# Kernel optimization log

Measured on AMD Instinct MI355X. Metric: run time of the kernel, lower is better.

## Reference

```python
import jax, jax.numpy as jnp
import numpy as np

DIM = 512
HEADS = 16
DIM_HEAD = 64
INNER = HEADS * DIM_HEAD
MAX_T = 32
BASE = 10000.0


def rotate_half(t):
    t1, t2 = jnp.split(t, 2, axis=-1)
    return jnp.concatenate((-t2, t1), axis=-1)


def setup_inputs() -> dict:
    key = jax.random.key(0)
    ks = jax.random.split(key, 12)
    B, T, S = 2, 16, 128
    x = jax.random.normal(ks[0], (B, T, S, DIM), dtype=jnp.float32)
    y = jax.random.normal(ks[1], (B, T, S, DIM), dtype=jnp.float32)
    temporal_mask = jax.random.randint(ks[2], (B, T, T), 0, 2).astype(jnp.int32)
    sc = 1.0 / np.sqrt(DIM)
    Wq = jax.random.normal(ks[3], (DIM, INNER), dtype=jnp.float32) * sc
    Wk = jax.random.normal(ks[4], (DIM, INNER), dtype=jnp.float32) * sc
    Wv = jax.random.normal(ks[5], (DIM, INNER), dtype=jnp.float32) * sc
    Wo = jax.random.normal(ks[6], (INNER, DIM), dtype=jnp.float32) / np.sqrt(INNER)
    bo = jnp.zeros((DIM,), dtype=jnp.float32)
    pos_emb = jax.random.normal(ks[7], (MAX_T, DIM), dtype=jnp.float32)
    gate_w = jax.random.normal(ks[8], (DIM, 1), dtype=jnp.float32) * sc
    gate_b = jnp.zeros((1,), dtype=jnp.float32)
    return {"x": x, "y": y, "temporal_mask": temporal_mask, "Wq": Wq, "Wk": Wk,
            "Wv": Wv, "Wo": Wo, "bo": bo, "pos_emb": pos_emb,
            "gate_w": gate_w, "gate_b": gate_b}


def reference(x, y, temporal_mask, Wq, Wk, Wv, Wo, bo, pos_emb, gate_w, gate_b):
    B, T, S, D = x.shape
    n = T * S
    scale = DIM_HEAD ** (-0.5)
    # temporal positional embedding (T <= MAX_T path)
    tp = pos_emb[:T][None, :, None, :]  # [1,T,1,D]
    x = x + tp
    y = y + tp
    xf = x.reshape(B, n, D)
    yf = y.reshape(B, n, D)
    # NOTE: k is computed from x (as in the source), v from y
    q = (xf @ Wq).reshape(B, n, HEADS, DIM_HEAD).transpose(0, 2, 1, 3)
    k = (xf @ Wk).reshape(B, n, HEADS, DIM_HEAD).transpose(0, 2, 1, 3)
    v = (yf @ Wv).reshape(B, n, HEADS, DIM_HEAD).transpose(0, 2, 1, 3)
    # RoPE over flattened token index
    inv_freq = 1.0 / (BASE ** (jnp.arange(0, DIM_HEAD, 2, dtype=jnp.float32) / DIM_HEAD))
    freqs = jnp.arange(n, dtype=jnp.float32)[:, None] * inv_freq[None, :]  # [n, d/2]
    emb = jnp.concatenate((freqs, freqs), axis=-1)  # [n, d]
    fc = jnp.cos(emb)[None, None, :, :]
    fs = jnp.sin(emb)[None, None, :, :]
    q = q * fc + rotate_half(q) * fs
    k = k * fc + rotate_half(k) * fs
    dots = jnp.einsum('bhid,bhjd->bhij', q, k) * scale  # [B,H,n,n]
    # expand temporal mask [B,T,T] -> [B,1,n,n] block structure
    m = jnp.repeat(jnp.repeat(temporal_mask, S, axis=1), S, axis=2)[:, None, :, :]
    dots = jnp.where(m == 0, -jnp.inf, dots)
    attn = jax.nn.softmax(dots, axis=-1)
    out = jnp.einsum('bhij,bhjd->bhid', attn, v)  # [B,H,n,d]
    out = out.transpose(0, 2, 1, 3).reshape(B, n, INNER)
    out = out @ Wo + bo
    out = out.reshape(B, T, S, D)
    gate = jax.nn.sigmoid(out @ gate_w + gate_b)  # [B,T,S,1]
    return out * gate
```

## Files before the change

### kernel.cpp

```cpp
#include <hip/hip_runtime.h>
#include <hip/hip_bf16.h>

typedef __attribute__((ext_vector_type(4))) short short4v;
typedef __attribute__((ext_vector_type(8))) short short8v;
typedef __attribute__((ext_vector_type(4))) float float4v;
typedef __attribute__((ext_vector_type(2))) unsigned int uint2v;
typedef __attribute__((ext_vector_type(4))) unsigned int uint4v;

#define NTOK 2048
#define MROWS 4096
#define DMODEL 512
#define NINNER 1024
#define DH 64
#define HH 16
#define LOG2E 1.4426950408889634f

__device__ __forceinline__ unsigned short b2s(float f) {
    __hip_bfloat16 h = __float2bfloat16(f);
    return __builtin_bit_cast(unsigned short, h);
}
__device__ __forceinline__ float bf2f(unsigned short h) {
    unsigned int u = ((unsigned int)h) << 16;
    return __builtin_bit_cast(float, u);
}

__device__ __forceinline__ float4v mfma32(short8v a, short8v b, float4v c) {
    return __builtin_amdgcn_mfma_f32_16x16x32_bf16(a, b, c, 0, 0, 0);
}

__device__ __forceinline__ void gld16(const void* g, void* l) {
    __builtin_amdgcn_global_load_lds((const __attribute__((address_space(1))) void*)g,
                                     (__attribute__((address_space(3))) void*)l, 16, 0, 0);
}

__global__ void k_pre(const float* __restrict__ x, const float* __restrict__ y,
                      const float* __restrict__ pe,
                      unsigned short* __restrict__ xpb, unsigned short* __restrict__ ypb,
                      const float* __restrict__ Wq, const float* __restrict__ Wk,
                      const float* __restrict__ Wv, const float* __restrict__ Wo,
                      const float* __restrict__ gwv, const float* __restrict__ gbv,
                      const float* __restrict__ bo,
                      unsigned short* __restrict__ wall, unsigned short* __restrict__ wot,
                      float* __restrict__ ctab, float* __restrict__ stab,
                      unsigned short* __restrict__ gvp, float* __restrict__ bgp) {
    __shared__ float tl[64][65];
    const int blk = blockIdx.x;
    const int tid = threadIdx.x;
    if (blk < 2048) {
        int e0 = (blk * 256 + tid) * 4;
        int row = e0 >> 9, col = e0 & 511;
        int t = (row & (NTOK - 1)) >> 7;
        const float4v xv = *(const float4v*)(x + e0);
        const float4v yv = *(const float4v*)(y + e0);
        const float4v pv = *(const float4v*)(pe + t * DMODEL + col);
        short4v xo, yo;
#pragma unroll
        for (int i = 0; i < 4; ++i) {
            xo[i] = (short)b2s(xv[i] + pv[i]);
            yo[i] = (short)b2s(yv[i] + pv[i]);
        }
        *(short4v*)(xpb + e0) = xo;
        *(short4v*)(ypb + e0) = yo;
    } else if (blk < 2560) {
        int t = blk - 2048;
        const float* W;
        unsigned short* dst;
        int K, N, k0, n0;
        if (t < 384) {
            int which = t / 128, tile = t % 128;
            W = (which == 0) ? Wq : (which == 1) ? Wk : Wv;
            dst = wall + (size_t)which * 1024 * 512;
            K = 512; N = 1024;
            k0 = (tile >> 4) * 64; n0 = (tile & 15) * 64;
        } else {
            int tile = t - 384;
            W = Wo; dst = wot;
            K = 1024; N = 512;
            k0 = (tile >> 3) * 64; n0 = (tile & 7) * 64;
        }
        int tx = tid & 63, ty4 = tid >> 6;
#pragma unroll
        for (int p = 0; p < 16; ++p) {
            int ky = p * 4 + ty4;
            tl[ky][tx] = W[(size_t)(k0 + ky) * N + n0 + tx];
        }
        __syncthreads();
#pragma unroll
        for (int p = 0; p < 16; ++p) {
            int ny = p * 4 + ty4;
            dst[(size_t)(n0 + ny) * K + k0 + tx] = b2s(tl[tx][ny]);
        }
    } else if (blk < 2816) {
        int idx = (blk - 2560) * 256 + tid;
        int p = idx >> 5, j = idx & 31;
        float invf = powf(10000.0f, -(float)(2 * j) * (1.0f / 64.0f));
        float f = (float)p * invf;
        ctab[idx] = cosf(f);
        stab[idx] = sinf(f);
    } else if (blk < 2832) {
        int base = (blk - 2816) * 64;
        int w = tid >> 6, l = tid & 63, l16 = l & 15, g = l >> 4;
        int row = base + w * 16 + l16;
        const float* wr = Wo + (size_t)row * 512 + g * 128;
        const float* gr = gwv + g * 128;
        float s = 0.f;
#pragma unroll
        for (int t = 0; t < 32; ++t) {
            float4v a = *(const float4v*)(wr + t * 4);
            float4v b = *(const float4v*)(gr + t * 4);
            s += a[0] * b[0] + a[1] * b[1] + a[2] * b[2] + a[3] * b[3];
        }
        s += __shfl_xor(s, 16);
        s += __shfl_xor(s, 32);
        if (g == 0) gvp[row] = b2s(s);
    } else {
        if (tid < 64) {
            float s = 0.f;
#pragma unroll
            for (int t = 0; t < 8; ++t) s += bo[tid + t * 64] * gwv[tid + t * 64];
#pragma unroll
            for (int off = 32; off > 0; off >>= 1) s += __shfl_xor(s, off);
            if (tid == 0) bgp[0] = s + gbv[0];
        }
    }
}

__global__ __launch_bounds__(256) void k_qkv(const unsigned short* __restrict__ A,
                                             const unsigned short* __restrict__ A2,
                                             const unsigned short* __restrict__ Bt,
                                             unsigned short* __restrict__ Cq,
                                             unsigned short* __restrict__ Ck,
                                             unsigned short* __restrict__ Cvv,
                                             const float* __restrict__ ctab,
                                             const float* __restrict__ stab,
                                             float scale) {
    __shared__ unsigned short Ab[2][4096];
    __shared__ unsigned short Bb[2][4096];
    const int tid = threadIdx.x;
    const int w = tid >> 6, l = tid & 63, l16 = l & 15, g = l >> 4;
    const int wm = w >> 1, wn = w & 1;
    const int m0 = blockIdx.y * 128, n0 = blockIdx.x * 128;
    const unsigned short* Ap = (n0 >= 2048) ? A2 : A;
    float4v acc[4][4];
#pragma unroll
    for (int i = 0; i < 4; ++i)
#pragma unroll
        for (int j = 0; j < 4; ++j) acc[i][j] = (float4v){0.f, 0.f, 0.f, 0.f};

    auto stage = [&](int t, int buf) {
        int k0 = t * 32;
#pragma unroll
        for (int it = 0; it < 2; ++it) {
            int f = it * 4 + w;
            gld16(Ap + (size_t)(m0 + f * 16 + l16) * 512 + k0 + g * 8, &Ab[buf][f * 512]);
            gld16(Bt + (size_t)(n0 + f * 16 + l16) * 512 + k0 + g * 8, &Bb[buf][f * 512]);
        }
    };

    stage(0, 0);
    __syncthreads();
    for (int t = 0; t < 16; ++t) {
        const int cur = t & 1;
        if (t + 1 < 16) stage(t + 1, cur ^ 1);
        short8v af[4], bf[4];
#pragma unroll
        for (int mi = 0; mi < 4; ++mi)
            af[mi] = *(const short8v*)&Ab[cur][(wm * 4 + mi) * 512 + l * 8];
#pragma unroll
        for (int nj = 0; nj < 4; ++nj)
            bf[nj] = *(const short8v*)&Bb[cur][(wn * 4 + nj) * 512 + l * 8];
        __builtin_amdgcn_s_setprio(1);
#pragma unroll
        for (int mi = 0; mi < 4; ++mi)
#pragma unroll
            for (int nj = 0; nj < 4; ++nj)
                acc[mi][nj] = mfma32(af[mi], bf[nj], acc[mi][nj]);
        __builtin_amdgcn_s_setprio(0);
        __syncthreads();
    }

    const int hh = (n0 + wn * 64) >> 6;
    const int head = hh & 15;
    if (hh < 32) {
        unsigned short* out = (hh < 16) ? Cq : Ck;
        const float sc = (hh < 16) ? scale : 1.0f;
#pragma unroll
        for (int mi = 0; mi < 4; ++mi)
#pragma unroll
            for (int r = 0; r < 4; ++r) {
                int row = m0 + wm * 64 + mi * 16 + g * 4 + r;
                int b = row >> 11, pos = row & (NTOK - 1);
                const float* cr = ctab + pos * 32;
                const float* sr = stab + pos * 32;
                unsigned short* ob = out + (size_t)((b * HH + head) * NTOK + pos) * DH;
#pragma unroll
                for (int nj = 0; nj < 2; ++nj) {
                    int j = nj * 16 + l16;
                    float c = cr[j], s = sr[j];
                    float v1 = acc[mi][nj][r], v2 = acc[mi][nj + 2][r];
                    ob[j] = b2s((v1 * c - v2 * s) * sc);
                    ob[j + 32] = b2s((v2 * c + v1 * s) * sc);
                }
            }
    } else {
#pragma unroll
        for (int mi = 0; mi < 4; ++mi)
#pragma unroll
            for (int nj = 0; nj < 4; ++nj) {
                int d = nj * 16 + l16;
                int row0 = m0 + wm * 64 + mi * 16 + g * 4;
                int b = row0 >> 11, pos0 = row0 & (NTOK - 1);
                short4v o;
#pragma unroll
                for (int r = 0; r < 4; ++r) o[r] = (short)b2s(acc[mi][nj][r]);
                *(short4v*)(Cvv + (size_t)((b * HH + head) * DH + d) * NTOK + pos0) = o;
            }
    }
}

__global__ __launch_bounds__(256) void k_gatev(const unsigned short* __restrict__ otm,
                                               const unsigned short* __restrict__ gv,
                                               const float* __restrict__ bgp,
                                               float* __restrict__ glog) {
    int row = blockIdx.x * 4 + (threadIdx.x >> 6);
    int l = threadIdx.x & 63;
    const unsigned short* pr = otm + (size_t)row * NINNER;
    float acc = 0.f;
#pragma unroll
    for (int c = 0; c < 2; ++c) {
        short8v a = *(const short8v*)(pr + (c * 64 + l) * 8);
        short8v b = *(const short8v*)(gv + (c * 64 + l) * 8);
#pragma unroll
        for (int j = 0; j < 8; ++j)
            acc = fmaf(bf2f((unsigned short)a[j]), bf2f((unsigned short)b[j]), acc);
    }
#pragma unroll
    for (int off = 32; off > 0; off >>= 1) acc += __shfl_xor(acc, off);
    if (l == 0) glog[row] = 1.0f / (1.0f + __expf(-(acc + bgp[0])));
}

__global__ __launch_bounds__(256) void k_oproj(const unsigned short* __restrict__ A,
                                               const unsigned short* __restrict__ Bt,
                                               const float* __restrict__ bo,
                                               const float* __restrict__ glog,
                                               float* __restrict__ out) {
    __shared__ unsigned short Ab[2][4096];
    __shared__ unsigned short Bb[2][2048];
    const int tid = threadIdx.x;
    const int w = tid >> 6, l = tid & 63, l16 = l & 15, g = l >> 4;
    const int m0 = blockIdx.y * 128, n0 = blockIdx.x * 64;
    float4v acc[2][4];
#pragma unroll
    for (int i = 0; i < 2; ++i)
#pragma unroll
        for (int j = 0; j < 4; ++j) acc[i][j] = (float4v){0.f, 0.f, 0.f, 0.f};

    auto stage = [&](int t, int buf) {
        int k0 = t * 32;
#pragma unroll
        for (int s = 0; s < 2; ++s) {
            int fi = s * 4 + w;
            gld16(A + (size_t)(m0 + fi * 16 + l16) * 1024 + k0 + g * 8, &Ab[buf][fi * 512]);
        }
        gld16(Bt + (size_t)(n0 + w * 16 + l16) * 1024 + k0 + g * 8, &Bb[buf][w * 512]);
    };

    stage(0, 0);
    __syncthreads();
    for (int t = 0; t < 32; ++t) {
        const int cur = t & 1;
        if (t + 1 < 32) stage(t + 1, cur ^ 1);
        short8v af[2], bf[4];
#pragma unroll
        for (int mi = 0; mi < 2; ++mi)
            af[mi] = *(const short8v*)&Ab[cur][(w * 2 + mi) * 512 + l * 8];
#pragma unroll
        for (int nj = 0; nj < 4; ++nj)
            bf[nj] = *(const short8v*)&Bb[cur][nj * 512 + l * 8];
        __builtin_amdgcn_s_setprio(1);
#pragma unroll
        for (int mi = 0; mi < 2; ++mi)
#pragma unroll
            for (int nj = 0; nj < 4; ++nj)
                acc[mi][nj] = mfma32(af[mi], bf[nj], acc[mi][nj]);
        __builtin_amdgcn_s_setprio(0);
        __syncthreads();
    }
#pragma unroll
    for (int mi = 0; mi < 2; ++mi) {
        float gl[4];
#pragma unroll
        for (int r = 0; r < 4; ++r)
            gl[r] = glog[m0 + w * 32 + mi * 16 + g * 4 + r];
#pragma unroll
        for (int nj = 0; nj < 4; ++nj) {
            int col = n0 + nj * 16 + l16;
            float bv = bo[col];
#pragma unroll
            for (int r = 0; r < 4; ++r) {
                int row = m0 + w * 32 + mi * 16 + g * 4 + r;
                out[(size_t)row * 512 + col] = (acc[mi][nj][r] + bv) * gl[r];
            }
        }
    }
}

__global__ __launch_bounds__(512) void k_attn(const unsigned short* __restrict__ qh,
                                              const unsigned short* __restrict__ kh,
                                              const unsigned short* __restrict__ vt,
                                              const int* __restrict__ tmask,
                                              unsigned short* __restrict__ otmp) {
    __shared__ unsigned short Kb[2][4096];
    __shared__ unsigned short Vb[2][4096];
    __shared__ int tlist[33];
    const int blk = blockIdx.x;
    const int u = (blk & 7) * 64 + (blk >> 3);
    const int ti = u & 15, h = (u >> 4) & 15, b = u >> 8;
    const int tid = threadIdx.x, w = tid >> 6, l = tid & 63, l16 = l & 15, g = l >> 4;
    if (tid == 0) {
        int c = 0;
        for (int j = 0; j < 16; ++j)
            if (tmask[(b * 16 + ti) * 16 + j]) { tlist[c++] = 2 * j; tlist[c++] = 2 * j + 1; }
        tlist[32] = c;
    }
    __syncthreads();
    const int cnt = tlist[32];
    const unsigned short* qb = qh + (size_t)((b * HH + h) * NTOK) * DH;
    const unsigned short* kb = kh + (size_t)((b * HH + h) * NTOK) * DH;
    const unsigned short* vb = vt + (size_t)((b * HH + h) * DH) * NTOK;
    const int q0 = ti * 128 + w * 16;

    short8v qf[2];
#pragma unroll
    for (int c = 0; c < 2; ++c)
        qf[c] = *(const short8v*)(qb + (size_t)(q0 + l16) * DH + c * 32 + g * 8);

    float4v oacc[4];
#pragma unroll
    for (int i = 0; i < 4; ++i) oacc[i] = (float4v){0.f, 0.f, 0.f, 0.f};
    float mx = -1e30f, lrow = 0.f;
    uint4v vrg;

    auto stageK = [&](int st, int buf) {
        const unsigned short* ga =
            kb + (size_t)(st * 64 + (w >> 1) * 16 + l16) * DH + (w & 1) * 32 + g * 8;
        gld16(ga, &Kb[buf][w * 512]);
    };
    auto loadV = [&](int st) {
        const unsigned short* ga =
            vb + (size_t)((w >> 1) * 16 + l16) * NTOK + st * 64 + (w & 1) * 32 + g * 4;
        uint2v lo = *(const uint2v*)ga;
        uint2v hi = *(const uint2v*)(ga + 16);
        vrg = (uint4v){lo[0], lo[1], hi[0], hi[1]};
    };
    auto writeV = [&](int buf) {
        *(uint4v*)&Vb[buf][w * 512 + l * 8] = vrg;
    };

    if (cnt > 0) {
        stageK(tlist[0], 0);
        loadV(tlist[0]);
        writeV(0);
        __syncthreads();
        for (int i = 0; i < cnt; ++i) {
            const int cur = i & 1;
            const bool pre = (i + 1 < cnt);
            if (pre) { stageK(tlist[i + 1], cur ^ 1); loadV(tlist[i + 1]); }
            float4v sacc[4];
#pragma unroll
            for (int jk = 0; jk < 4; ++jk) sacc[jk] = (float4v){0.f, 0.f, 0.f, 0.f};
            __builtin_amdgcn_s_setprio(1);
#pragma unroll
            for (int jk = 0; jk < 4; ++jk) {
                short8v kf0 = *(const short8v*)&Kb[cur][(jk * 2 + 0) * 512 + l * 8];
                short8v kf1 = *(const short8v*)&Kb[cur][(jk * 2 + 1) * 512 + l * 8];
                sacc[jk] = mfma32(kf0, qf[0], sacc[jk]);
                sacc[jk] = mfma32(kf1, qf[1], sacc[jk]);
            }
            __builtin_amdgcn_s_setprio(0);
            float tm = -1e30f;
#pragma unroll
            for (int jk = 0; jk < 4; ++jk) {
                float4v s4 = sacc[jk];
                tm = fmaxf(tm, fmaxf(fmaxf(s4[0], s4[1]), fmaxf(s4[2], s4[3])));
            }
            tm = fmaxf(tm, __shfl_xor(tm, 16));
            tm = fmaxf(tm, __shfl_xor(tm, 32));
            if (!__all(tm <= mx + 8.0f)) {
                float mnew = fmaxf(mx, tm);
                float alpha = exp2f(mx - mnew);
                lrow *= alpha;
#pragma unroll
                for (int md = 0; md < 4; ++md)
#pragma unroll
                    for (int r = 0; r < 4; ++r) oacc[md][r] *= alpha;
                mx = mnew;
            }
            short8v pf[2];
            float4v tsv = {0.f, 0.f, 0.f, 0.f};
#pragma unroll
            for (int cc = 0; cc < 2; ++cc) {
                float p[8];
#pragma unroll
                for (int r = 0; r < 4; ++r) {
                    p[r] = exp2f(sacc[2 * cc][r] - mx);
                    p[r + 4] = exp2f(sacc[2 * cc + 1][r] - mx);
                }
                short8v pv;
#pragma unroll
                for (int r = 0; r < 4; ++r) {
                    tsv[r] += p[r] + p[r + 4];
                    pv[r] = (short)b2s(p[r]);
                    pv[r + 4] = (short)b2s(p[r + 4]);
                }
                pf[cc] = pv;
            }
            float ts = (tsv[0] + tsv[1]) + (tsv[2] + tsv[3]);
            ts += __shfl_xor(ts, 16);
            ts += __shfl_xor(ts, 32);
            lrow += ts;
            if (pre) writeV(cur ^ 1);
            __builtin_amdgcn_s_setprio(1);
#pragma unroll
            for (int md = 0; md < 4; ++md)
#pragma unroll
                for (int cc = 0; cc < 2; ++cc) {
                    short8v vf = *(const short8v*)&Vb[cur][(md * 2 + cc) * 512 + l * 8];
                    oacc[md] = mfma32(vf, pf[cc], oacc[md]);
                }
            __builtin_amdgcn_s_setprio(0);
            __syncthreads();
        }
    }
    float inv = lrow > 0.f ? 1.0f / lrow : 0.f;
    int q = q0 + l16;
#pragma unroll
    for (int md = 0; md < 4; ++md) {
        short4v o;
#pragma unroll
        for (int r = 0; r < 4; ++r) o[r] = (short)b2s(oacc[md][r] * inv);
        *(short4v*)(otmp + (size_t)(b * NTOK + q) * NINNER + h * DH + md * 16 + g * 4) = o;
    }
}

extern "C" void kernel_launch(void* const* d_in, const int* in_sizes, int n_in,
                              void* d_out, int out_size, void* d_ws, size_t ws_size,
                              hipStream_t stream) {
    (void)in_sizes; (void)n_in; (void)out_size; (void)ws_size;
    const float* x = (const float*)d_in[0];
    const float* y = (const float*)d_in[1];
    const int* tmask = (const int*)d_in[2];
    const float* Wq = (const float*)d_in[3];
    const float* Wk = (const float*)d_in[4];
    const float* Wv = (const float*)d_in[5];
    const float* Wo = (const float*)d_in[6];
    const float* bo = (const float*)d_in[7];
    const float* pe = (const float*)d_in[8];
    const float* gw = (const float*)d_in[9];
    const float* gb = (const float*)d_in[10];

    char* ws = (char*)d_ws;
    const size_t MB = 1u << 20;
    unsigned short* xpb  = (unsigned short*)(ws + 0);
    unsigned short* ypb  = (unsigned short*)(ws + 4 * MB);
    unsigned short* wall = (unsigned short*)(ws + 8 * MB);
    unsigned short* wot  = (unsigned short*)(ws + 11 * MB);
    unsigned short* qh   = (unsigned short*)(ws + 12 * MB);
    unsigned short* kh   = (unsigned short*)(ws + 20 * MB);
    unsigned short* vt   = (unsigned short*)(ws + 28 * MB);
    unsigned short* otm  = (unsigned short*)(ws + 36 * MB);
    float* ct = (float*)(ws + 44 * MB);
    float* st = (float*)(ws + 44 * MB + 256 * 1024);
    unsigned short* gv = (unsigned short*)(ws + 45 * MB);
    float* bg = (float*)(ws + 45 * MB + 4096);
    float* glog = (float*)(ws + 45 * MB + 8192);
    float* outp = (float*)d_out;

    k_pre<<<2833, 256, 0, stream>>>(x, y, pe, xpb, ypb, Wq, Wk, Wv, Wo, gw, gb, bo,
                                    wall, wot, ct, st, gv, bg);
    k_qkv<<<dim3(24, 32), 256, 0, stream>>>(xpb, ypb, wall, qh, kh, vt, ct, st,
                                            0.125f * LOG2E);
    k_attn<<<512, 512, 0, stream>>>(qh, kh, vt, tmask, otm);
    k_gatev<<<1024, 256, 0, stream>>>(otm, gv, bg, glog);
    k_oproj<<<dim3(8, 32), 256, 0, stream>>>(otm, wot, bo, glog, outp);
}
```

Before: 133.0 us.

## Halve attention block size and compute row sums with an MFMA against ones

The attention kernel now runs 1024 blocks of 256 threads, each covering half of a 128-query tile, instead of 512 blocks of 512 threads. Each wave therefore stages two K/V fragments per step. The softmax denominator is no longer built from float adds and cross-lane shuffles; it comes from an extra MFMA that multiplies a vector of bf16 ones by the probability fragments. The intent is more blocks for scheduling and less VALU and shuffle work, at the cost of loading K/V twice across the two half-blocks and summing bf16-rounded probabilities for the normaliser.

```diff
diff --git a/kernel.cpp b/kernel.cpp
--- a/kernel.cpp
+++ b/kernel.cpp
@@ -305,7 +305,7 @@
     }
 }
 
-__global__ __launch_bounds__(512) void k_attn(const unsigned short* __restrict__ qh,
+__global__ __launch_bounds__(256) void k_attn(const unsigned short* __restrict__ qh,
                                               const unsigned short* __restrict__ kh,
                                               const unsigned short* __restrict__ vt,
                                               const int* __restrict__ tmask,
@@ -314,8 +314,8 @@
     __shared__ unsigned short Vb[2][4096];
     __shared__ int tlist[33];
     const int blk = blockIdx.x;
-    const int u = (blk & 7) * 64 + (blk >> 3);
-    const int ti = u & 15, h = (u >> 4) & 15, b = u >> 8;
+    const int u = (blk & 7) * 128 + (blk >> 3);
+    const int half = u & 1, ti = (u >> 1) & 15, h = (u >> 5) & 15, b = u >> 9;
     const int tid = threadIdx.x, w = tid >> 6, l = tid & 63, l16 = l & 15, g = l >> 4;
     if (tid == 0) {
         int c = 0;
@@ -328,33 +328,48 @@
     const unsigned short* qb = qh + (size_t)((b * HH + h) * NTOK) * DH;
     const unsigned short* kb = kh + (size_t)((b * HH + h) * NTOK) * DH;
     const unsigned short* vb = vt + (size_t)((b * HH + h) * DH) * NTOK;
-    const int q0 = ti * 128 + w * 16;
+    const int q0 = ti * 128 + half * 64 + w * 16;
 
     short8v qf[2];
 #pragma unroll
     for (int c = 0; c < 2; ++c)
         qf[c] = *(const short8v*)(qb + (size_t)(q0 + l16) * DH + c * 32 + g * 8);
 
+    short8v ones;
+#pragma unroll
+    for (int j = 0; j < 8; ++j) ones[j] = (short)0x3F80;
+
     float4v oacc[4];
 #pragma unroll
     for (int i = 0; i < 4; ++i) oacc[i] = (float4v){0.f, 0.f, 0.f, 0.f};
-    float mx = -1e30f, lrow = 0.f;
-    uint4v vrg;
+    float4v lsum = (float4v){0.f, 0.f, 0.f, 0.f};
+    float mx = -1e30f;
+    uint4v vrg[2];
 
     auto stageK = [&](int st, int buf) {
-        const unsigned short* ga =
-            kb + (size_t)(st * 64 + (w >> 1) * 16 + l16) * DH + (w & 1) * 32 + g * 8;
-        gld16(ga, &Kb[buf][w * 512]);
+#pragma unroll
+        for (int s = 0; s < 2; ++s) {
+            int fi = w * 2 + s;
+            const unsigned short* ga =
+                kb + (size_t)(st * 64 + (fi >> 1) * 16 + l16) * DH + (fi & 1) * 32 + g * 8;
+            gld16(ga, &Kb[buf][fi * 512]);
+        }
     };
     auto loadV = [&](int st) {
-        const unsigned short* ga =
-            vb + (size_t)((w >> 1) * 16 + l16) * NTOK + st * 64 + (w & 1) * 32 + g * 4;
-        uint2v lo = *(const uint2v*)ga;
-        uint2v hi = *(const uint2v*)(ga + 16);
-        vrg = (uint4v){lo[0], lo[1], hi[0], hi[1]};
+#pragma unroll
+        for (int s = 0; s < 2; ++s) {
+            int fi = w * 2 + s;
+            const unsigned short* ga =
+                vb + (size_t)((fi >> 1) * 16 + l16) * NTOK + st * 64 + (fi & 1) * 32 + g * 4;
+            uint2v lo = *(const uint2v*)ga;
+            uint2v hi = *(const uint2v*)(ga + 16);
+            vrg[s] = (uint4v){lo[0], lo[1], hi[0], hi[1]};
+        }
     };
     auto writeV = [&](int buf) {
-        *(uint4v*)&Vb[buf][w * 512 + l * 8] = vrg;
+#pragma unroll
+        for (int s = 0; s < 2; ++s)
+            *(uint4v*)&Vb[buf][(w * 2 + s) * 512 + l * 8] = vrg[s];
     };
 
     if (cnt > 0) {
@@ -389,7 +404,8 @@
             if (!__all(tm <= mx + 8.0f)) {
                 float mnew = fmaxf(mx, tm);
                 float alpha = exp2f(mx - mnew);
-                lrow *= alpha;
+#pragma unroll
+                for (int r = 0; r < 4; ++r) lsum[r] *= alpha;
 #pragma unroll
                 for (int md = 0; md < 4; ++md)
 #pragma unroll
@@ -397,30 +413,20 @@
                 mx = mnew;
             }
             short8v pf[2];
-            float4v tsv = {0.f, 0.f, 0.f, 0.f};
 #pragma unroll
             for (int cc = 0; cc < 2; ++cc) {
-                float p[8];
+                short8v pv;
 #pragma unroll
                 for (int r = 0; r < 4; ++r) {
-                    p[r] = exp2f(sacc[2 * cc][r] - mx);
-                    p[r + 4] = exp2f(sacc[2 * cc + 1][r] - mx);
-                }
-                short8v pv;
-#pragma unroll
-                for (int r = 0; r < 4; ++r) {
-                    tsv[r] += p[r] + p[r + 4];
-                    pv[r] = (short)b2s(p[r]);
-                    pv[r + 4] = (short)b2s(p[r + 4]);
+                    pv[r] = (short)b2s(exp2f(sacc[2 * cc][r] - mx));
+                    pv[r + 4] = (short)b2s(exp2f(sacc[2 * cc + 1][r] - mx));
                 }
                 pf[cc] = pv;
             }
-            float ts = (tsv[0] + tsv[1]) + (tsv[2] + tsv[3]);
-            ts += __shfl_xor(ts, 16);
-            ts += __shfl_xor(ts, 32);
-            lrow += ts;
             if (pre) writeV(cur ^ 1);
             __builtin_amdgcn_s_setprio(1);
+#pragma unroll
+            for (int cc = 0; cc < 2; ++cc) lsum = mfma32(ones, pf[cc], lsum);
 #pragma unroll
             for (int md = 0; md < 4; ++md)
 #pragma unroll
@@ -432,6 +438,7 @@
             __syncthreads();
         }
     }
+    float lrow = lsum[0];
     float inv = lrow > 0.f ? 1.0f / lrow : 0.f;
     int q = q0 + l16;
 #pragma unroll
@@ -480,7 +487,7 @@
                                     wall, wot, ct, st, gv, bg);
     k_qkv<<<dim3(24, 32), 256, 0, stream>>>(xpb, ypb, wall, qh, kh, vt, ct, st,
                                             0.125f * LOG2E);
-    k_attn<<<512, 512, 0, stream>>>(qh, kh, vt, tmask, otm);
+    k_attn<<<1024, 256, 0, stream>>>(qh, kh, vt, tmask, otm);
     k_gatev<<<1024, 256, 0, stream>>>(otm, gv, bg, glog);
     k_oproj<<<dim3(8, 32), 256, 0, stream>>>(otm, wot, bo, glog, outp);
 }
```

Result: slower. 146.3 us (+10.0%).

## Software-pipeline QK^T one tile ahead and compute row sums via MFMA

Applied to the files above, without the earlier changes.

Restructures the attention loop so the QK^T MFMAs for the next key tile are issued while softmax for the current tile runs. K staging gets a third LDS buffer and is prefetched two tiles ahead. It also replaces the shuffle-based row-sum reduction with an MFMA against a ones vector, which accumulates the softmax denominator in the matrix unit. The cost is more registers from holding two score sets and more LDS from the third K buffer, which could lower occupancy.

```diff
diff --git a/kernel.cpp b/kernel.cpp
--- a/kernel.cpp
+++ b/kernel.cpp
@@ -310,7 +310,7 @@
                                               const unsigned short* __restrict__ vt,
                                               const int* __restrict__ tmask,
                                               unsigned short* __restrict__ otmp) {
-    __shared__ unsigned short Kb[2][4096];
+    __shared__ unsigned short Kb[3][4096];
     __shared__ unsigned short Vb[2][4096];
     __shared__ int tlist[33];
     const int blk = blockIdx.x;
@@ -335,11 +335,17 @@
     for (int c = 0; c < 2; ++c)
         qf[c] = *(const short8v*)(qb + (size_t)(q0 + l16) * DH + c * 32 + g * 8);
 
+    short8v ones;
+#pragma unroll
+    for (int j = 0; j < 8; ++j) ones[j] = (short)0x3F80;
+
     float4v oacc[4];
 #pragma unroll
     for (int i = 0; i < 4; ++i) oacc[i] = (float4v){0.f, 0.f, 0.f, 0.f};
-    float mx = -1e30f, lrow = 0.f;
+    float4v lsum = (float4v){0.f, 0.f, 0.f, 0.f};
+    float mx = -1e30f;
     uint4v vrg;
+    float4v sA[4], sB[4];
 
     auto stageK = [&](int st, int buf) {
         const unsigned short* ga =
@@ -356,82 +362,83 @@
     auto writeV = [&](int buf) {
         *(uint4v*)&Vb[buf][w * 512 + l * 8] = vrg;
     };
+    auto qkcomp = [&](int buf, float4v (&s)[4]) {
+#pragma unroll
+        for (int jk = 0; jk < 4; ++jk) s[jk] = (float4v){0.f, 0.f, 0.f, 0.f};
+        __builtin_amdgcn_s_setprio(1);
+#pragma unroll
+        for (int jk = 0; jk < 4; ++jk) {
+            short8v kf0 = *(const short8v*)&Kb[buf][(jk * 2 + 0) * 512 + l * 8];
+            short8v kf1 = *(const short8v*)&Kb[buf][(jk * 2 + 1) * 512 + l * 8];
+            s[jk] = mfma32(kf0, qf[0], s[jk]);
+            s[jk] = mfma32(kf1, qf[1], s[jk]);
+        }
+        __builtin_amdgcn_s_setprio(0);
+    };
+
+    auto body = [&](int i, float4v (&scur)[4], float4v (&snext)[4]) {
+        const bool pre1 = (i + 1 < cnt), pre2 = (i + 2 < cnt);
+        if (pre2) stageK(tlist[i + 2], (i + 2) % 3);
+        if (pre1) loadV(tlist[i + 1]);
+        float tm = -1e30f;
+#pragma unroll
+        for (int jk = 0; jk < 4; ++jk) {
+            float4v s4 = scur[jk];
+            tm = fmaxf(tm, fmaxf(fmaxf(s4[0], s4[1]), fmaxf(s4[2], s4[3])));
+        }
+        tm = fmaxf(tm, __shfl_xor(tm, 16));
+        tm = fmaxf(tm, __shfl_xor(tm, 32));
+        if (!__all(tm <= mx + 8.0f)) {
+            float mnew = fmaxf(mx, tm);
+            float alpha = exp2f(mx - mnew);
+#pragma unroll
+            for (int r = 0; r < 4; ++r) lsum[r] *= alpha;
+#pragma unroll
+            for (int md = 0; md < 4; ++md)
+#pragma unroll
+                for (int r = 0; r < 4; ++r) oacc[md][r] *= alpha;
+            mx = mnew;
+        }
+        if (pre1) qkcomp((i + 1) % 3, snext);
+        short8v pf[2];
+#pragma unroll
+        for (int cc = 0; cc < 2; ++cc) {
+            short8v pv;
+#pragma unroll
+            for (int r = 0; r < 4; ++r) {
+                pv[r] = (short)b2s(exp2f(scur[2 * cc][r] - mx));
+                pv[r + 4] = (short)b2s(exp2f(scur[2 * cc + 1][r] - mx));
+            }
+            pf[cc] = pv;
+        }
+        __builtin_amdgcn_s_setprio(1);
+#pragma unroll
+        for (int cc = 0; cc < 2; ++cc) lsum = mfma32(ones, pf[cc], lsum);
+#pragma unroll
+        for (int md = 0; md < 4; ++md)
+#pragma unroll
+            for (int cc = 0; cc < 2; ++cc) {
+                short8v vf = *(const short8v*)&Vb[i & 1][(md * 2 + cc) * 512 + l * 8];
+                oacc[md] = mfma32(vf, pf[cc], oacc[md]);
+            }
+        __builtin_amdgcn_s_setprio(0);
+        if (pre1) writeV((i + 1) & 1);
+        __syncthreads();
+    };
 
     if (cnt > 0) {
         stageK(tlist[0], 0);
         loadV(tlist[0]);
+        if (cnt > 1) stageK(tlist[1], 1);
         writeV(0);
         __syncthreads();
-        for (int i = 0; i < cnt; ++i) {
-            const int cur = i & 1;
-            const bool pre = (i + 1 < cnt);
-            if (pre) { stageK(tlist[i + 1], cur ^ 1); loadV(tlist[i + 1]); }
-            float4v sacc[4];
-#pragma unroll
-            for (int jk = 0; jk < 4; ++jk) sacc[jk] = (float4v){0.f, 0.f, 0.f, 0.f};
-            __builtin_amdgcn_s_setprio(1);
-#pragma unroll
-            for (int jk = 0; jk < 4; ++jk) {
-                short8v kf0 = *(const short8v*)&Kb[cur][(jk * 2 + 0) * 512 + l * 8];
-                short8v kf1 = *(const short8v*)&Kb[cur][(jk * 2 + 1) * 512 + l * 8];
-                sacc[jk] = mfma32(kf0, qf[0], sacc[jk]);
-                sacc[jk] = mfma32(kf1, qf[1], sacc[jk]);
-            }
-            __builtin_amdgcn_s_setprio(0);
-            float tm = -1e30f;
-#pragma unroll
-            for (int jk = 0; jk < 4; ++jk) {
-                float4v s4 = sacc[jk];
-                tm = fmaxf(tm, fmaxf(fmaxf(s4[0], s4[1]), fmaxf(s4[2], s4[3])));
-            }
-            tm = fmaxf(tm, __shfl_xor(tm, 16));
-            tm = fmaxf(tm, __shfl_xor(tm, 32));
-            if (!__all(tm <= mx + 8.0f)) {
-                float mnew = fmaxf(mx, tm);
-                float alpha = exp2f(mx - mnew);
-                lrow *= alpha;
-#pragma unroll
-                for (int md = 0; md < 4; ++md)
-#pragma unroll
-                    for (int r = 0; r < 4; ++r) oacc[md][r] *= alpha;
-                mx = mnew;
-            }
-            short8v pf[2];
-            float4v tsv = {0.f, 0.f, 0.f, 0.f};
-#pragma unroll
-            for (int cc = 0; cc < 2; ++cc) {
-                float p[8];
-#pragma unroll
-                for (int r = 0; r < 4; ++r) {
-                    p[r] = exp2f(sacc[2 * cc][r] - mx);
-                    p[r + 4] = exp2f(sacc[2 * cc + 1][r] - mx);
-                }
-                short8v pv;
-#pragma unroll
-                for (int r = 0; r < 4; ++r) {
-                    tsv[r] += p[r] + p[r + 4];
-                    pv[r] = (short)b2s(p[r]);
-                    pv[r + 4] = (short)b2s(p[r + 4]);
-                }
-                pf[cc] = pv;
-            }
-            float ts = (tsv[0] + tsv[1]) + (tsv[2] + tsv[3]);
-            ts += __shfl_xor(ts, 16);
-            ts += __shfl_xor(ts, 32);
-            lrow += ts;
-            if (pre) writeV(cur ^ 1);
-            __builtin_amdgcn_s_setprio(1);
-#pragma unroll
-            for (int md = 0; md < 4; ++md)
-#pragma unroll
-                for (int cc = 0; cc < 2; ++cc) {
-                    short8v vf = *(const short8v*)&Vb[cur][(md * 2 + cc) * 512 + l * 8];
-                    oacc[md] = mfma32(vf, pf[cc], oacc[md]);
-                }
-            __builtin_amdgcn_s_setprio(0);
-            __syncthreads();
-        }
-    }
+        qkcomp(0, sA);
+        for (int i = 0; i < cnt; i += 2) {
+            body(i, sA, sB);
+            if (i + 1 < cnt) body(i + 1, sB, sA);
+        }
+    }
+    float lrow = lsum[0];
     float inv = lrow > 0.f ? 1.0f / lrow : 0.f;
     int q = q0 + l16;
 #pragma unroll
```

Result: faster. 123.7 us (-7.0%).
